# Performance work log

Measured on AMD Instinct MI355X. Metric: run time of the kernel, lower is better.

## Reference

```python
import jax, jax.numpy as jnp
import numpy as np

N, NFEAT, NHID1, NHID2 = 16384, 128, 128, 64

def setup_inputs() -> dict:
    key = jax.random.key(0)
    k1, k2, k3, k4 = jax.random.split(key, 4)
    feature = jax.random.normal(k1, (N, NFEAT), dtype=jnp.float32)
    # dense (row-normalized) adjacency surrogate
    adj = jax.random.uniform(k2, (N, N), dtype=jnp.float32) / N
    W1 = jax.random.normal(k3, (NFEAT, NHID1), dtype=jnp.float32) / np.sqrt(NFEAT)
    b1 = jnp.zeros((NHID1,), dtype=jnp.float32)
    W2 = jax.random.normal(k4, (NHID1, NHID2), dtype=jnp.float32) / np.sqrt(NHID1)
    b2 = jnp.zeros((NHID2,), dtype=jnp.float32)
    return {"feature": feature, "adj": adj, "W1": W1, "b1": b1, "W2": W2, "b2": b2}

def reference(feature, adj, W1, b1, W2, b2):
    # layer 1: support = X@W1; agg = A@support; relu
    h = jax.nn.relu(adj @ (feature @ W1) + b1)
    # dropout is identity in eval mode
    # layer 2
    out = adj @ (h @ W2) + b2
    return out
```

## Files before the change

### kernel.cpp

```cpp
#include <hip/hip_runtime.h>
#include <stdint.h>

typedef float  f32x4  __attribute__((ext_vector_type(4)));
typedef short  short8 __attribute__((ext_vector_type(8)));
typedef __bf16 bf16x8 __attribute__((ext_vector_type(8)));

__device__ __forceinline__ unsigned short f2bf(float f) {
    unsigned u = __builtin_bit_cast(unsigned, f);
    unsigned r = u + 0x7fffu + ((u >> 16) & 1u);
    return (unsigned short)(r >> 16);
}

__device__ __forceinline__ short8 cvt8(f32x4 a, f32x4 b) {
    short8 r;
    r[0] = (short)f2bf(a[0]); r[1] = (short)f2bf(a[1]);
    r[2] = (short)f2bf(a[2]); r[3] = (short)f2bf(a[3]);
    r[4] = (short)f2bf(b[0]); r[5] = (short)f2bf(b[1]);
    r[6] = (short)f2bf(b[2]); r[7] = (short)f2bf(b[3]);
    return r;
}

typedef const __attribute__((address_space(1))) void* gas_p;
typedef __attribute__((address_space(3))) void*       las_p;
__device__ __forceinline__ void gld_lds16(const void* g, void* l) {
    __builtin_amdgcn_global_load_lds((gas_p)g, (las_p)l, 16, 0, 0);
}

__device__ __forceinline__ f32x4 mfma16(short8 a, short8 b, f32x4 c) {
    return __builtin_amdgcn_mfma_f32_16x16x32_bf16(
        __builtin_bit_cast(bf16x8, a), __builtin_bit_cast(bf16x8, b), c, 0, 0, 0);
}

template<int NMAT>
__global__ __launch_bounds__(256) void k_xw_t(const float* __restrict__ X,
                                              const float* __restrict__ W,
                                              short* __restrict__ St, int M) {
    constexpr int K   = 128;
    constexpr int NPT = NMAT / 4;
    __shared__ float Xs[64][129];
    __shared__ float Ws[K][NMAT];

    const int tid = threadIdx.x;
    const int m0  = blockIdx.x * 64;

    constexpr int WCH = K * NMAT / 4 / 256;
    #pragma unroll
    for (int j = 0; j < WCH; ++j) {
        int ch = tid + j * 256;
        ((float4*)Ws)[ch] = ((const float4*)W)[ch];
    }
    #pragma unroll
    for (int j = 0; j < 8; ++j) {
        int ch = tid + j * 256;
        int r = ch >> 5, c4 = ch & 31;
        float4 v = *(const float4*)(X + (size_t)(m0 + r) * K + c4 * 4);
        Xs[r][c4 * 4 + 0] = v.x; Xs[r][c4 * 4 + 1] = v.y;
        Xs[r][c4 * 4 + 2] = v.z; Xs[r][c4 * 4 + 3] = v.w;
    }
    __syncthreads();

    const int m  = tid & 63;
    const int n0 = (tid >> 6) * NPT;
    float acc[NPT];
    #pragma unroll
    for (int i = 0; i < NPT; ++i) acc[i] = 0.f;

    for (int k = 0; k < K; ++k) {
        float x = Xs[m][k];
        #pragma unroll
        for (int i = 0; i < NPT; i += 4) {
            float4 w = *(const float4*)&Ws[k][n0 + i];
            acc[i + 0] += x * w.x; acc[i + 1] += x * w.y;
            acc[i + 2] += x * w.z; acc[i + 3] += x * w.w;
        }
    }
    #pragma unroll
    for (int i = 0; i < NPT; ++i)
        St[(size_t)(n0 + i) * M + m0 + m] = (short)f2bf(acc[i]);
}

template<int BN, bool RELU>
__global__ __launch_bounds__(256, 2) void k_adj_gemm(const float* __restrict__ A,
                                                     const short* __restrict__ Bt,
                                                     const float* __restrict__ bias,
                                                     float* __restrict__ out,
                                                     int M, int K) {
    constexpr int BM    = 64, BK = 64;
    constexpr int NF    = BN / 16;
    constexpr int BCH   = BN * BK * 2 / (256 * 16);
    constexpr int VMCNT = BCH + 4;

    __shared__ short Bs[3][BN * 64];

    const int tid  = threadIdx.x;
    const int wave = tid >> 6, lane = tid & 63;
    const int lr   = lane & 15, lk = lane >> 4;
    const int row0 = blockIdx.x * BM;
    const int row_g = row0 + wave * 16 + lr;

    const char* Abase = (const char*)A + (size_t)row_g * K * 4 + lk * 32;

    const int key   = (lr & 7) << 4;
    const int offs0 = (lk * 16) ^ key;
    const int offs1 = (64 + lk * 16) ^ key;

    f32x4 acc[NF];
    #pragma unroll
    for (int n = 0; n < NF; ++n) acc[n] = (f32x4)0.f;

    f32x4 a0[4], a1[4];
    const int NT  = K / BK;
    const int NTM = NT - 1;
    const int kt0 = (blockIdx.x * 97) & NTM;

#define LOAD_A(SLOT, KTP)                                                       \
    {                                                                           \
        const char* p = Abase + (size_t)(KTP) * 256;                            \
        SLOT[0] = *(const f32x4*)(p);                                           \
        SLOT[1] = *(const f32x4*)(p + 16);                                      \
        SLOT[2] = *(const f32x4*)(p + 128);                                     \
        SLOT[3] = *(const f32x4*)(p + 144);                                     \
    }
#define STAGE_B(BUF, KTP)                                                       \
    {                                                                           \
        _Pragma("unroll")                                                       \
        for (int j = 0; j < BCH; ++j) {                                         \
            int o = (tid + j * 256) * 16;          \
            int r = o >> 7, w = o & 127;                                        \
            const char* src = (const char*)Bt + (size_t)r * (K * 2)             \
                              + (size_t)(KTP) * 128 + (w ^ ((r & 7) << 4));     \
            gld_lds16(src, (char*)&Bs[BUF][0] + o);                             \
        }                                                                       \
    }

    LOAD_A(a0, kt0)
    LOAD_A(a1, (kt0 + 1) & NTM)
    STAGE_B(0, kt0)

#define ITER(KT, SA, CB, NB)                                                    \
    {                                                                           \
           \
        short8 fa0 = cvt8(SA[0], SA[1]);                                        \
        short8 fa1 = cvt8(SA[2], SA[3]);                                        \
          \
        { int kta = ((KT) + 2 + kt0) & NTM; LOAD_A(SA, kta) }                   \
        { int ktn = ((KT) + 1 + kt0) & NTM; STAGE_B(NB, ktn) }                  \
        __builtin_amdgcn_sched_barrier(0);                                      \
                     \
        asm volatile("s_waitcnt vmcnt(%0)" :: "i"(VMCNT) : "memory");           \
        __builtin_amdgcn_s_barrier();                     \
        __builtin_amdgcn_sched_barrier(0);                                      \
                                       \
        _Pragma("unroll")                                                       \
        for (int n = 0; n < NF; ++n) {                                          \
            short8 b0 = *(const short8*)((const char*)&Bs[CB][0]                \
                                         + n * 2048 + lr * 128 + offs0);        \
            acc[n] = mfma16(fa0, b0, acc[n]);                                   \
            short8 b1 = *(const short8*)((const char*)&Bs[CB][0]                \
                                         + n * 2048 + lr * 128 + offs1);        \
            acc[n] = mfma16(fa1, b1, acc[n]);                                   \
        }                                                                       \
    }

    for (int g = 0; g < 42; ++g) {
        int t = g * 6;
        ITER(t + 0, a0, 0, 1)
        ITER(t + 1, a1, 1, 2)
        ITER(t + 2, a0, 2, 0)
        ITER(t + 3, a1, 0, 1)
        ITER(t + 4, a0, 1, 2)
        ITER(t + 5, a1, 2, 0)
    }
    ITER(252, a0, 0, 1)
    ITER(253, a1, 1, 2)
    ITER(254, a0, 2, 0)
    ITER(255, a1, 0, 1)
#undef ITER
#undef LOAD_A
#undef STAGE_B

    #pragma unroll
    for (int n = 0; n < NF; ++n) {
        int col = n * 16 + lr;
        float bv = bias[col];
        #pragma unroll
        for (int j = 0; j < 4; ++j) {
            int row = row0 + wave * 16 + lk * 4 + j;
            float v = acc[n][j] + bv;
            if (RELU) v = fmaxf(v, 0.f);
            out[(size_t)row * BN + col] = v;
        }
    }
}

extern "C" void kernel_launch(void* const* d_in, const int* in_sizes, int n_in,
                              void* d_out, int out_size, void* d_ws, size_t ws_size,
                              hipStream_t stream) {
    const int N = 16384, NH1 = 128, NH2 = 64;
    const float* feature = (const float*)d_in[0];
    const float* adj     = (const float*)d_in[1];
    const float* W1      = (const float*)d_in[2];
    const float* b1      = (const float*)d_in[3];
    const float* W2      = (const float*)d_in[4];
    const float* b2      = (const float*)d_in[5];

    short* S1t = (short*)d_ws;
    float* h   = (float*)((char*)d_ws + (4u << 20));
    short* S2t = (short*)((char*)d_ws + (12u << 20));

    k_xw_t<NH1><<<N / 64, 256, 0, stream>>>(feature, W1, S1t, N);
    k_adj_gemm<NH1, true ><<<N / 64, 256, 0, stream>>>(adj, S1t, b1, h, N, N);
    k_xw_t<NH2><<<N / 64, 256, 0, stream>>>(h, W2, S2t, N);
    k_adj_gemm<NH2, false><<<N / 64, 256, 0, stream>>>(adj, S2t, b2, (float*)d_out, N, N);
    (void)in_sizes; (void)n_in; (void)out_size; (void)ws_size;
}
```

Measured before the change: 565.0 us.

## Batch A loads four tiles deep and use four-stage LDS ring for B

The adjacency GEMM now loads A fragments in batches of four K-tiles into two register banks, double-buffered, instead of two single-tile slots. B staging moves to a four-buffer LDS ring, and the wait counts vary per iteration to match the batched loads. Occupancy drops to one block per SIMD to make room for the extra registers, and the per-block staggered K start offset is removed. The aim is deeper memory-latency hiding for the bandwidth-bound adjacency stream. The cost is fewer resident waves, and with every block starting at the same K tile, DRAM channel contention may rise.

```diff
diff --git a/kernel.cpp b/kernel.cpp
--- a/kernel.cpp
+++ b/kernel.cpp
@@ -80,17 +80,18 @@
 }
 
 template<int BN, bool RELU>
-__global__ __launch_bounds__(256, 2) void k_adj_gemm(const float* __restrict__ A,
+__global__ __launch_bounds__(256, 1) void k_adj_gemm(const float* __restrict__ A,
                                                      const short* __restrict__ Bt,
                                                      const float* __restrict__ bias,
                                                      float* __restrict__ out,
                                                      int M, int K) {
-    constexpr int BM    = 64, BK = 64;
-    constexpr int NF    = BN / 16;
-    constexpr int BCH   = BN * BK * 2 / (256 * 16);
-    constexpr int VMCNT = BCH + 4;
-
-    __shared__ short Bs[3][BN * 64];
+    constexpr int BM   = 64, BK = 64;
+    constexpr int NF   = BN / 16;
+    constexpr int BCH  = BN * BK * 2 / (256 * 16);
+    constexpr int VMH  = BCH + 16;
+    constexpr int VML  = BCH;
+
+    __shared__ short Bs[4][BN * 64];
 
     const int tid  = threadIdx.x;
     const int wave = tid >> 6, lane = tid & 63;
@@ -108,18 +109,24 @@
     #pragma unroll
     for (int n = 0; n < NF; ++n) acc[n] = (f32x4)0.f;
 
-    f32x4 a0[4], a1[4];
+    f32x4 bA0[16], bA1[16];
     const int NT  = K / BK;
     const int NTM = NT - 1;
-    const int kt0 = (blockIdx.x * 97) & NTM;
-
-#define LOAD_A(SLOT, KTP)                                                       \
-    {                                                                           \
-        const char* p = Abase + (size_t)(KTP) * 256;                            \
-        SLOT[0] = *(const f32x4*)(p);                                           \
-        SLOT[1] = *(const f32x4*)(p + 16);                                      \
-        SLOT[2] = *(const f32x4*)(p + 128);                                     \
-        SLOT[3] = *(const f32x4*)(p + 144);                                     \
+
+#define LOAD_SLOT(QARR, BI, TT)                                                 \
+    {                                                                           \
+        const char* p = Abase + (size_t)(TT) * 256;                             \
+        QARR[(BI) + 0] = *(const f32x4*)(p);                                    \
+        QARR[(BI) + 1] = *(const f32x4*)(p + 16);                               \
+        QARR[(BI) + 2] = *(const f32x4*)(p + 128);                              \
+        QARR[(BI) + 3] = *(const f32x4*)(p + 144);                              \
+    }
+#define LOAD_BATCH(QARR, T0)                                                    \
+    {                                                                           \
+        LOAD_SLOT(QARR, 0,  ((T0) + 0) & NTM)                                   \
+        LOAD_SLOT(QARR, 4,  ((T0) + 1) & NTM)                                   \
+        LOAD_SLOT(QARR, 8,  ((T0) + 2) & NTM)                                   \
+        LOAD_SLOT(QARR, 12, ((T0) + 3) & NTM)                                   \
     }
 #define STAGE_B(BUF, KTP)                                                       \
     {                                                                           \
@@ -133,24 +140,22 @@
         }                                                                       \
     }
 
-    LOAD_A(a0, kt0)
-    LOAD_A(a1, (kt0 + 1) & NTM)
-    STAGE_B(0, kt0)
-
-#define ITER(KT, SA, CB, NB)                                                    \
-    {                                                                           \
-           \
-        short8 fa0 = cvt8(SA[0], SA[1]);                                        \
-        short8 fa1 = cvt8(SA[2], SA[3]);                                        \
-          \
-        { int kta = ((KT) + 2 + kt0) & NTM; LOAD_A(SA, kta) }                   \
-        { int ktn = ((KT) + 1 + kt0) & NTM; STAGE_B(NB, ktn) }                  \
+    LOAD_BATCH(bA0, 0)
+    STAGE_B(0, 0)
+    LOAD_BATCH(bA1, 4)
+
+#define ITER(KT, QARR, J4, CB, NB, VM, BATCH_STMT)                              \
+    {                                                                           \
+                        \
+        short8 fa0 = cvt8(QARR[(J4) + 0], QARR[(J4) + 1]);                      \
+        short8 fa1 = cvt8(QARR[(J4) + 2], QARR[(J4) + 3]);                      \
+        { int ktn = ((KT) + 1) & NTM; STAGE_B(NB, ktn) }                        \
+        BATCH_STMT                                                              \
         __builtin_amdgcn_sched_barrier(0);                                      \
-                     \
-        asm volatile("s_waitcnt vmcnt(%0)" :: "i"(VMCNT) : "memory");           \
+            \
+        asm volatile("s_waitcnt vmcnt(%0)" :: "i"(VM) : "memory");              \
         __builtin_amdgcn_s_barrier();                     \
         __builtin_amdgcn_sched_barrier(0);                                      \
-                                       \
         _Pragma("unroll")                                                       \
         for (int n = 0; n < NF; ++n) {                                          \
             short8 b0 = *(const short8*)((const char*)&Bs[CB][0]                \
@@ -162,21 +167,20 @@
         }                                                                       \
     }
 
-    for (int g = 0; g < 42; ++g) {
-        int t = g * 6;
-        ITER(t + 0, a0, 0, 1)
-        ITER(t + 1, a1, 1, 2)
-        ITER(t + 2, a0, 2, 0)
-        ITER(t + 3, a1, 0, 1)
-        ITER(t + 4, a0, 1, 2)
-        ITER(t + 5, a1, 2, 0)
-    }
-    ITER(252, a0, 0, 1)
-    ITER(253, a1, 1, 2)
-    ITER(254, a0, 2, 0)
-    ITER(255, a1, 0, 1)
+    for (int g = 0; g < 32; ++g) {
+        int t = g * 8;
+        ITER(t + 0, bA0, 0,  0, 1, VMH, )
+        ITER(t + 1, bA0, 4,  1, 2, VML, )
+        ITER(t + 2, bA0, 8,  2, 3, VML, )
+        ITER(t + 3, bA0, 12, 3, 0, VMH, LOAD_BATCH(bA0, (t + 3) + 5))
+        ITER(t + 4, bA1, 0,  0, 1, VMH, )
+        ITER(t + 5, bA1, 4,  1, 2, VML, )
+        ITER(t + 6, bA1, 8,  2, 3, VML, )
+        ITER(t + 7, bA1, 12, 3, 0, VMH, LOAD_BATCH(bA1, (t + 7) + 5))
+    }
 #undef ITER
-#undef LOAD_A
+#undef LOAD_BATCH
+#undef LOAD_SLOT
 #undef STAGE_B
 
     #pragma unroll
```

Result: faster. 486.8 us (-13.8%).
